# Kernel optimization log

Hardware: AMD Instinct MI355X
Metric: run time of the kernel (lower is better)

Reference implementation:

```python
import jax, jax.numpy as jnp
import numpy as np

N_KERNELS = 16
KSIZE = 3
B, H, W = 16, 512, 512

def setup_inputs() -> dict:
    key = jax.random.key(0)
    k1, k2, k3, k4 = jax.random.split(key, 4)
    x = jax.random.uniform(k1, (B, 1, H, W), dtype=jnp.float32)
    kernels = jax.random.normal(k2, (N_KERNELS, 1, KSIZE, KSIZE), dtype=jnp.float32)
    reactants = jax.random.normal(k3, (N_KERNELS,), dtype=jnp.float32)
    products = jax.random.normal(k4, (N_KERNELS,), dtype=jnp.float32)
    return {"x": x, "kernels": kernels, "reactants": reactants, "products": products}

def reference(x, kernels, reactants, products):
    # All n_kernels 1->1 convs batched as a single 1->n_kernels conv.
    pad = KSIZE // 2
    N = jax.lax.conv_general_dilated(
        x, kernels,
        window_strides=(1, 1),
        padding=[(pad, pad), (pad, pad)],
        dimension_numbers=("NCHW", "OIHW", "NCHW"),
    )  # [B, n_kernels, H, W]
    GAIN = 10.0
    condition = jax.nn.sigmoid(GAIN * (N - reactants[None, :, None, None]))
    # x has 1 channel; broadcasts against the n_kernels axis
    update = condition * (products[None, :, None, None] - x)
    delta = jnp.sum(update, axis=1, keepdims=True)  # sum over kernels -> [B,1,H,W]
    return jnp.clip(x + delta, 0.0, 1.0)
```

## Files before the change

kernel.cpp:

```cpp
#include <hip/hip_runtime.h>


#define NK 16
#define BATCH 16
#define H 512
#define W 512
#define G2 14.4269504088896340f

typedef float f2 __attribute__((ext_vector_type(2)));

#if __has_builtin(__builtin_amdgcn_exp2f)
#define EXP2F(x) __builtin_amdgcn_exp2f(x)
#else
#define EXP2F(x) exp2f(x)
#endif

#if __has_builtin(__builtin_elementwise_fma)
#define FMA2(a, b, c) __builtin_elementwise_fma((a), (b), (c))
#else
#define FMA2(a, b, c) ((a) * (b) + (c))
#endif

static __device__ __forceinline__ f2 bc2(float s) { f2 r; r.x = s; r.y = s; return r; }

typedef const __attribute__((address_space(4))) float cfloat;

__global__ __launch_bounds__(256, 4) void nca_kernel(
    const float* __restrict__ x,
    const float* __restrict__ kernels,
    const float* __restrict__ reactants,
    const float* __restrict__ products,
    float* __restrict__ out)
{
    const int idx = blockIdx.x * blockDim.x + threadIdx.x;
    const int w4 = (idx & 127) << 2;
    const int h0 = ((idx >> 7) & 255) << 1;
    const int b  = idx >> 15;

    const float* xb = x + (size_t)b * (H * W);

    float v[4][6];
#pragma unroll
    for (int r = 0; r < 4; ++r) {
        const int row = h0 + r - 1;
        if (row >= 0 && row < H) {
            const float* xr = xb + row * W;
            const float4 c = *(const float4*)(xr + w4);
            v[r][1] = c.x; v[r][2] = c.y; v[r][3] = c.z; v[r][4] = c.w;
            v[r][0] = (w4 > 0)     ? xr[w4 - 1] : 0.0f;
            v[r][5] = (w4 + 4 < W) ? xr[w4 + 4] : 0.0f;
        } else {
#pragma unroll
            for (int c = 0; c < 6; ++c) v[r][c] = 0.0f;
        }
    }

    f2 sl[4][5];
#pragma unroll
    for (int r = 0; r < 4; ++r)
#pragma unroll
        for (int s = 0; s < 5; ++s) { sl[r][s].x = v[r][s]; sl[r][s].y = v[r][s + 1]; }

    cfloat* kc = (cfloat*)kernels;
    cfloat* rc = (cfloat*)reactants;
    cfloat* pc = (cfloat*)products;

    f2 s0[2][2], s1[2][2];
#pragma unroll
    for (int py = 0; py < 2; ++py)
#pragma unroll
        for (int g = 0; g < 2; ++g) { s0[py][g] = bc2(0.0f); s1[py][g] = bc2(0.0f); }

    const f2 mg2 = bc2(-G2);
    const f2 one = bc2(1.0f);

#pragma unroll
    for (int k = 0; k < NK; ++k) {
        f2 wk[9];
#pragma unroll
        for (int i = 0; i < 9; ++i) wk[i] = bc2(kc[k * 9 + i]);
        const f2 c2 = bc2(G2 * rc[k]);
        const f2 pk = bc2(pc[k]);

#pragma unroll
        for (int py = 0; py < 2; ++py) {
#pragma unroll
            for (int g = 0; g < 2; ++g) {
                f2 n = bc2(0.0f);
#pragma unroll
                for (int r = 0; r < 3; ++r)
#pragma unroll
                    for (int c = 0; c < 3; ++c)
                        n = FMA2(sl[py + r][2 * g + c], wk[r * 3 + c], n);
                const f2 z = FMA2(mg2, n, c2);
                f2 e;
                e.x = EXP2F(z.x);
                e.y = EXP2F(z.y);
                const f2 d = e + one;
                f2 sig;
                sig.x = __builtin_amdgcn_rcpf(d.x);
                sig.y = __builtin_amdgcn_rcpf(d.y);
                s0[py][g] = s0[py][g] + sig;
                s1[py][g] = FMA2(sig, pk, s1[py][g]);
            }
        }
    }

#pragma unroll
    for (int py = 0; py < 2; ++py) {
        float4 o;
#pragma unroll
        for (int g = 0; g < 2; ++g) {
            const f2 xv = sl[py + 1][2 * g + 1];
            f2 res = FMA2(-xv, s0[py][g], xv + s1[py][g]);
            res.x = fminf(fmaxf(res.x, 0.0f), 1.0f);
            res.y = fminf(fmaxf(res.y, 0.0f), 1.0f);
            if (g == 0) { o.x = res.x; o.y = res.y; }
            else        { o.z = res.x; o.w = res.y; }
        }
        *(float4*)(out + ((size_t)(b * H + h0 + py) * W + w4)) = o;
    }
}

extern "C" void kernel_launch(void* const* d_in, const int* in_sizes, int n_in,
                              void* d_out, int out_size, void* d_ws, size_t ws_size,
                              hipStream_t stream) {
    const float* x         = (const float*)d_in[0];
    const float* kernels   = (const float*)d_in[1];
    const float* reactants = (const float*)d_in[2];
    const float* products  = (const float*)d_in[3];
    float* out = (float*)d_out;

    const int total_tiles = BATCH * (H / 2) * (W / 4);
    nca_kernel<<<total_tiles / 256, 256, 0, stream>>>(x, kernels, reactants, products, out);
}
```

Before: 91.29 us.

## Prescale weights in prep kernel and shrink per-thread tile to 2x2

Adds a tiny prep kernel that writes the weights, reactant and product constants into the workspace as duplicated float2 pairs, with the -gain*log2e scale folded into the weights. The main kernel can then load packed pairs directly and drops one FMA per sigmoid. The per-thread tile shrinks from 2x4 to 2x2 pixels and the launch bound rises to 8 waves, trading more redundant halo loads and more threads for lower register pressure and higher occupancy. An extra kernel launch is added to every call.

```diff
diff --git a/kernel.cpp b/kernel.cpp
--- a/kernel.cpp
+++ b/kernel.cpp
@@ -23,102 +23,100 @@
 
 static __device__ __forceinline__ f2 bc2(float s) { f2 r; r.x = s; r.y = s; return r; }
 
-typedef const __attribute__((address_space(4))) float cfloat;
+typedef const __attribute__((address_space(4))) f2 cf2;
 
-__global__ __launch_bounds__(256, 4) void nca_kernel(
+__global__ void nca_prep(const float* __restrict__ kernels,
+                         const float* __restrict__ reactants,
+                         const float* __restrict__ products,
+                         float2* __restrict__ cw)
+{
+    const int t = threadIdx.x;
+    if (t < NK * 11) {
+        const int k = t / 11;
+        const int j = t % 11;
+        float v;
+        if (j < 9)        v = -G2 * kernels[k * 9 + j];
+        else if (j == 9)  v =  G2 * reactants[k];
+        else              v =  products[k];
+        cw[t] = make_float2(v, v);
+    }
+}
+
+__global__ __launch_bounds__(256, 8) void nca_kernel(
     const float* __restrict__ x,
-    const float* __restrict__ kernels,
-    const float* __restrict__ reactants,
-    const float* __restrict__ products,
+    const float2* __restrict__ cw_,
     float* __restrict__ out)
 {
     const int idx = blockIdx.x * blockDim.x + threadIdx.x;
-    const int w4 = (idx & 127) << 2;
-    const int h0 = ((idx >> 7) & 255) << 1;
-    const int b  = idx >> 15;
+    const int w2 = (idx & 255) << 1;
+    const int h0 = ((idx >> 8) & 255) << 1;
+    const int b  = idx >> 16;
 
     const float* xb = x + (size_t)b * (H * W);
 
-    float v[4][6];
+    f2 sl[4][3];
 #pragma unroll
     for (int r = 0; r < 4; ++r) {
         const int row = h0 + r - 1;
         if (row >= 0 && row < H) {
             const float* xr = xb + row * W;
-            const float4 c = *(const float4*)(xr + w4);
-            v[r][1] = c.x; v[r][2] = c.y; v[r][3] = c.z; v[r][4] = c.w;
-            v[r][0] = (w4 > 0)     ? xr[w4 - 1] : 0.0f;
-            v[r][5] = (w4 + 4 < W) ? xr[w4 + 4] : 0.0f;
+            const float2 c = *(const float2*)(xr + w2);
+            const float lft = (w2 > 0)     ? xr[w2 - 1] : 0.0f;
+            const float rgt = (w2 + 2 < W) ? xr[w2 + 2] : 0.0f;
+            sl[r][0].x = lft; sl[r][0].y = c.x;
+            sl[r][1].x = c.x; sl[r][1].y = c.y;
+            sl[r][2].x = c.y; sl[r][2].y = rgt;
         } else {
 #pragma unroll
-            for (int c = 0; c < 6; ++c) v[r][c] = 0.0f;
+            for (int c = 0; c < 3; ++c) sl[r][c] = bc2(0.0f);
         }
     }
 
-    f2 sl[4][5];
-#pragma unroll
-    for (int r = 0; r < 4; ++r)
-#pragma unroll
-        for (int s = 0; s < 5; ++s) { sl[r][s].x = v[r][s]; sl[r][s].y = v[r][s + 1]; }
+    cf2* cw = (cf2*)cw_;
 
-    cfloat* kc = (cfloat*)kernels;
-    cfloat* rc = (cfloat*)reactants;
-    cfloat* pc = (cfloat*)products;
+    f2 s0[2], s1[2];
+    s0[0] = bc2(0.0f); s0[1] = bc2(0.0f);
+    s1[0] = bc2(0.0f); s1[1] = bc2(0.0f);
 
-    f2 s0[2][2], s1[2][2];
-#pragma unroll
-    for (int py = 0; py < 2; ++py)
-#pragma unroll
-        for (int g = 0; g < 2; ++g) { s0[py][g] = bc2(0.0f); s1[py][g] = bc2(0.0f); }
-
-    const f2 mg2 = bc2(-G2);
     const f2 one = bc2(1.0f);
 
 #pragma unroll
     for (int k = 0; k < NK; ++k) {
         f2 wk[9];
 #pragma unroll
-        for (int i = 0; i < 9; ++i) wk[i] = bc2(kc[k * 9 + i]);
-        const f2 c2 = bc2(G2 * rc[k]);
-        const f2 pk = bc2(pc[k]);
+        for (int i = 0; i < 9; ++i) wk[i] = cw[k * 11 + i];
+        const f2 c2 = cw[k * 11 + 9];
+        const f2 pk = cw[k * 11 + 10];
 
 #pragma unroll
         for (int py = 0; py < 2; ++py) {
+            f2 n = bc2(0.0f);
 #pragma unroll
-            for (int g = 0; g < 2; ++g) {
-                f2 n = bc2(0.0f);
+            for (int r = 0; r < 3; ++r)
 #pragma unroll
-                for (int r = 0; r < 3; ++r)
-#pragma unroll
-                    for (int c = 0; c < 3; ++c)
-                        n = FMA2(sl[py + r][2 * g + c], wk[r * 3 + c], n);
-                const f2 z = FMA2(mg2, n, c2);
-                f2 e;
-                e.x = EXP2F(z.x);
-                e.y = EXP2F(z.y);
-                const f2 d = e + one;
-                f2 sig;
-                sig.x = __builtin_amdgcn_rcpf(d.x);
-                sig.y = __builtin_amdgcn_rcpf(d.y);
-                s0[py][g] = s0[py][g] + sig;
-                s1[py][g] = FMA2(sig, pk, s1[py][g]);
-            }
+                for (int c = 0; c < 3; ++c)
+                    n = FMA2(sl[py + r][c], wk[r * 3 + c], n);
+            const f2 z = n + c2;
+            f2 e;
+            e.x = EXP2F(z.x);
+            e.y = EXP2F(z.y);
+            const f2 d = e + one;
+            f2 sig;
+            sig.x = __builtin_amdgcn_rcpf(d.x);
+            sig.y = __builtin_amdgcn_rcpf(d.y);
+            s0[py] = s0[py] + sig;
+            s1[py] = FMA2(sig, pk, s1[py]);
         }
     }
 
 #pragma unroll
     for (int py = 0; py < 2; ++py) {
-        float4 o;
-#pragma unroll
-        for (int g = 0; g < 2; ++g) {
-            const f2 xv = sl[py + 1][2 * g + 1];
-            f2 res = FMA2(-xv, s0[py][g], xv + s1[py][g]);
-            res.x = fminf(fmaxf(res.x, 0.0f), 1.0f);
-            res.y = fminf(fmaxf(res.y, 0.0f), 1.0f);
-            if (g == 0) { o.x = res.x; o.y = res.y; }
-            else        { o.z = res.x; o.w = res.y; }
-        }
-        *(float4*)(out + ((size_t)(b * H + h0 + py) * W + w4)) = o;
+        const f2 xv = sl[py + 1][1];
+        f2 res = FMA2(-xv, s0[py], xv + s1[py]);
+        res.x = fminf(fmaxf(res.x, 0.0f), 1.0f);
+        res.y = fminf(fmaxf(res.y, 0.0f), 1.0f);
+        *(float2*)(out + ((size_t)(b * H + h0 + py) * W + w2)) =
+            make_float2(res.x, res.y);
     }
 }
 
@@ -130,7 +128,10 @@
     const float* reactants = (const float*)d_in[2];
     const float* products  = (const float*)d_in[3];
     float* out = (float*)d_out;
+    float2* cw = (float2*)d_ws;
 
-    const int total_tiles = BATCH * (H / 2) * (W / 4);
-    nca_kernel<<<total_tiles / 256, 256, 0, stream>>>(x, kernels, reactants, products, out);
+    nca_prep<<<1, 192, 0, stream>>>(kernels, reactants, products, cw);
+
+    const int total_tiles = BATCH * (H / 2) * (W / 2);
+    nca_kernel<<<total_tiles / 256, 256, 0, stream>>>(x, cw, out);
 }
```

Result: slower. 94.85 us (+3.9%).
